# Kernel tuning notes

Hardware: AMD Instinct MI355X
Metric: run time of the kernel (lower is better)

## Reference

```python
import jax, jax.numpy as jnp
import numpy as np
from jax import lax

T, B, D, H = 256, 32, 768, 768


def setup_inputs() -> dict:
    key = jax.random.key(0)
    ks = jax.random.split(key, 8)
    s = 1.0 / np.sqrt(H)
    x = jax.random.normal(ks[0], (T, B, D), dtype=jnp.float32)
    h0 = jax.random.normal(ks[1], (2, B, H), dtype=jnp.float32) * s
    wih_f = jax.random.normal(ks[2], (3 * H, D), dtype=jnp.float32) * s
    whh_f = jax.random.normal(ks[3], (3 * H, H), dtype=jnp.float32) * s
    wih_b = jax.random.normal(ks[4], (3 * H, D), dtype=jnp.float32) * s
    whh_b = jax.random.normal(ks[5], (3 * H, H), dtype=jnp.float32) * s
    bih_f = jnp.zeros((3 * H,), jnp.float32)
    bhh_f = jnp.zeros((3 * H,), jnp.float32)
    bih_b = jnp.zeros((3 * H,), jnp.float32)
    bhh_b = jnp.zeros((3 * H,), jnp.float32)
    # sorted-descending lengths in [T//2, T], as PackedSequence requires
    lengths = jnp.sort(jax.random.randint(ks[6], (B,), T // 2, T + 1))[::-1].astype(jnp.int32)
    return dict(x=x, h0=h0, wih_f=wih_f, whh_f=whh_f, bih_f=bih_f, bhh_f=bhh_f,
                wih_b=wih_b, whh_b=whh_b, bih_b=bih_b, bhh_b=bhh_b, lengths=lengths)


def _gru_scan(x_seq, h0d, Wih, Whh, bih, bhh, mask):
    """Masked GRU scan. x_seq [T,B,D], mask [T,B] bool; hidden frozen where mask is False
    (equivalent to PackedSequence shrinking/growing the active batch)."""
    def step(h, inp):
        x_t, m = inp  # [B,D], [B]
        gx = x_t @ Wih.T + bih          # [B,3H]
        gh = h @ Whh.T + bhh            # [B,3H]
        xr, xz, xn = jnp.split(gx, 3, axis=-1)
        hr, hz, hn = jnp.split(gh, 3, axis=-1)
        r = jax.nn.sigmoid(xr + hr)
        z = jax.nn.sigmoid(xz + hz)
        n = jnp.tanh(xn + r * hn)
        h_new = (1.0 - z) * n + z * h
        h_new = jnp.where(m[:, None], h_new, h)
        return h_new, h_new * m[:, None]  # zero outputs at padded positions
    h_last, outs = lax.scan(step, h0d, (x_seq, mask))
    return outs, h_last


def reference(x, h0, wih_f, whh_f, bih_f, bhh_f, wih_b, whh_b, bih_b, bhh_b, lengths):
    t_idx = jnp.arange(T)[:, None]                 # [T,1]
    mask = t_idx < lengths[None, :]                # [T,B]
    # forward direction
    out_f, h_f = _gru_scan(x, h0[0], wih_f, whh_f, bih_f, bhh_f, mask)
    # reverse direction: flip time, run, flip back
    out_b_rev, h_b = _gru_scan(x[::-1], h0[1], wih_b, whh_b, bih_b, bhh_b, mask[::-1])
    out_b = out_b_rev[::-1]
    outputs = jnp.concatenate([out_f, out_b], axis=-1)  # [T,B,2H], zero beyond length
    h_out = jnp.stack([h_f, h_b], axis=0)                # [2,B,H]
    return outputs, h_out
```

## Files before the change

### kernel.cpp

```cpp
#include <hip/hip_runtime.h>
#include <stdint.h>

typedef unsigned short u16;
typedef _Float16 f16;
typedef __attribute__((ext_vector_type(8))) _Float16 f16x8;
typedef __attribute__((ext_vector_type(4))) float f32x4;
typedef __attribute__((ext_vector_type(4))) unsigned short u16x4;

#define T_SEQ  256
#define BATCH  32
#define DIM    768
#define HID    768
#define G3     2304
#define N_ALL  4608
#define NSLICE 48
#define NBLK   96
#define FLAG_STRIDE 32

__device__ __forceinline__ u16 f2h(float f) {
  return __builtin_bit_cast(u16, (f16)f);
}
__device__ __forceinline__ float h2f(u16 h) {
  return (float)__builtin_bit_cast(f16, h);
}

__device__ __forceinline__ f16x8 load_coh16(const u16* p) {
  f16x8 v;
  asm volatile("global_load_dwordx4 %0, %1, off sc0 sc1" : "=v"(v) : "v"(p));
  return v;
}
__device__ __forceinline__ void store_coh16(u16* p, f16x8 v) {
  asm volatile("global_store_dwordx4 %0, %1, off sc0 sc1" :: "v"(p), "v"(v));
}
__device__ __forceinline__ void wait_vm0() {
  asm volatile("s_waitcnt vmcnt(0)" ::: "memory");
}

__global__ void k_cvt(const float* __restrict__ in, u16* __restrict__ out, int n4) {
  int i = blockIdx.x * blockDim.x + threadIdx.x;
  if (i >= n4) return;
  float4 v = ((const float4*)in)[i];
  u16x4 o;
  o[0] = f2h(v.x); o[1] = f2h(v.y); o[2] = f2h(v.z); o[3] = f2h(v.w);
  ((u16x4*)out)[i] = o;
}

__global__ void k_zero(int* p, int n) {
  int i = blockIdx.x * blockDim.x + threadIdx.x;
  if (i < n) p[i] = 0;
}

__global__ __launch_bounds__(256) void k_gemm(
    const u16* __restrict__ A, const u16* __restrict__ Bw,
    const float* __restrict__ bihf, const float* __restrict__ bihb,
    u16* __restrict__ gx)
{
  __shared__ __align__(16) u16 As[128 * 32];
  __shared__ __align__(16) u16 Bs[128 * 32];
  const int tid  = threadIdx.x;
  const int lane = tid & 63, wave = tid >> 6;
  const int wm = wave >> 1, wn = wave & 1;
  const int m0 = blockIdx.y * 128;
  const int n0 = blockIdx.x * 128;
  const int lr = lane & 15, lk = lane >> 4;
  f32x4 acc[4][4] = {};
  for (int k0 = 0; k0 < DIM; k0 += 32) {
    __syncthreads();
    #pragma unroll
    for (int i = 0; i < 2; ++i) {
      int c = i * 256 + tid;
      int row = c >> 2, kk = (c & 3) * 8;
      *(f16x8*)&As[c * 8] = *(const f16x8*)&A [(size_t)(m0 + row) * DIM + k0 + kk];
      *(f16x8*)&Bs[c * 8] = *(const f16x8*)&Bw[(size_t)(n0 + row) * DIM + k0 + kk];
    }
    __syncthreads();
    f16x8 af[4], bfr[4];
    #pragma unroll
    for (int f = 0; f < 4; ++f) {
      af[f]  = *(const f16x8*)&As[(wm * 64 + f * 16 + lr) * 32 + lk * 8];
      bfr[f] = *(const f16x8*)&Bs[(wn * 64 + f * 16 + lr) * 32 + lk * 8];
    }
    #pragma unroll
    for (int fm = 0; fm < 4; ++fm)
      #pragma unroll
      for (int fn = 0; fn < 4; ++fn)
        acc[fm][fn] = __builtin_amdgcn_mfma_f32_16x16x32_f16(af[fm], bfr[fn], acc[fm][fn], 0, 0, 0);
  }
  #pragma unroll
  for (int fm = 0; fm < 4; ++fm)
    #pragma unroll
    for (int fn = 0; fn < 4; ++fn) {
      int n = n0 + wn * 64 + fn * 16 + lr;
      float bias = (n < G3) ? bihf[n] : bihb[n - G3];
      #pragma unroll
      for (int r = 0; r < 4; ++r) {
        int m = m0 + wm * 64 + fm * 16 + lk * 4 + r;
        gx[(size_t)m * N_ALL + n] = f2h(acc[fm][fn][r] + bias);
      }
    }
}

__global__ __launch_bounds__(256, 1) void k_gru(
    const u16* __restrict__ whh,
    const u16* __restrict__ gx,
    const float* __restrict__ h0,
    const float* __restrict__ bhhf, const float* __restrict__ bhhb,
    const int* __restrict__ lengths,
    u16* __restrict__ hbuf,
    float* __restrict__ out, int* __restrict__ flags)
{
  const int blk   = blockIdx.x;
  const int dir   = blk / NSLICE;
  const int slice = blk % NSLICE;
  const int hbase = slice * 16;
  const int tid = threadIdx.x, lane = tid & 63, wave = tid >> 6;
  const int lr = lane & 15, lk = lane >> 4;
  const int c = hbase + lr;
  const int pollid = tid - 128;
  __shared__ __align__(16) float part[3][2][3][64][4];
  __shared__ __align__(16) u16 hx[32][16];

  f16x8 bw[3][6];
  #pragma unroll
  for (int g = 0; g < 3; ++g)
    #pragma unroll
    for (int ks = 0; ks < 6; ++ks)
      bw[g][ks] = *(const f16x8*)&whh[(size_t)(dir * G3 + g * HID + hbase + lr) * HID
                                      + wave * 192 + ks * 32 + lk * 8];

  float hst[2][4];
  float bh[3] = {0.f, 0.f, 0.f};
  int lenv[2][4];
  u16 g0[2][4], g1[2][4], g2[2][4];
  if (wave == 0) {
    #pragma unroll
    for (int m = 0; m < 2; ++m)
      #pragma unroll
      for (int r = 0; r < 4; ++r) {
        int b = m * 16 + lk * 4 + r;
        float h = h0[(size_t)dir * BATCH * HID + (size_t)b * HID + c];
        hst[m][r] = h;
        lenv[m][r] = lengths[b];
        hx[b][lr] = f2h(h);
      }
    const float* bhp = dir ? bhhb : bhhf;
    #pragma unroll
    for (int g = 0; g < 3; ++g) bh[g] = bhp[g * HID + c];
    asm volatile("s_waitcnt lgkmcnt(0)" ::: "memory");
    {
      f16x8 hv = *(const f16x8*)&hx[lane >> 1][(lane & 1) * 8];
      store_coh16(&hbuf[(size_t)(dir * BATCH + (lane >> 1)) * HID + hbase + (lane & 1) * 8], hv);
    }
    wait_vm0();
    if (lane == 0)
      __hip_atomic_store(&flags[blk * FLAG_STRIDE], 1, __ATOMIC_RELAXED, __HIP_MEMORY_SCOPE_AGENT);
    int t0 = dir ? (T_SEQ - 1) : 0;
    #pragma unroll
    for (int m = 0; m < 2; ++m)
      #pragma unroll
      for (int r = 0; r < 4; ++r) {
        int b = m * 16 + lk * 4 + r;
        size_t off = ((size_t)t0 * BATCH + b) * N_ALL + dir * G3 + c;
        g0[m][r] = gx[off]; g1[m][r] = gx[off + HID]; g2[m][r] = gx[off + 2 * HID];
      }
  }
  if (pollid >= 0 && pollid < NSLICE) {
    const int watch = (dir * NSLICE + pollid) * FLAG_STRIDE;
    while (__hip_atomic_load(&flags[watch], __ATOMIC_RELAXED, __HIP_MEMORY_SCOPE_AGENT) < 1)
      __builtin_amdgcn_s_sleep(1);
  }
  __syncthreads();

  for (int s = 0; s < T_SEQ; ++s) {
    const int par = s & 1;
    const int t = dir ? (T_SEQ - 1 - s) : s;
    const u16* hb = hbuf + (size_t)(par * 2 + dir) * BATCH * HID;
    f16x8 ah[2][6];
    #pragma unroll
    for (int m = 0; m < 2; ++m)
      #pragma unroll
      for (int ks = 0; ks < 6; ++ks)
        ah[m][ks] = load_coh16(&hb[(size_t)(m * 16 + lr) * HID + wave * 192 + ks * 32 + lk * 8]);
    wait_vm0();
    __builtin_amdgcn_sched_barrier(0);
    f32x4 acc[2][3] = {};
    #pragma unroll
    for (int ks = 0; ks < 6; ++ks)
      #pragma unroll
      for (int m = 0; m < 2; ++m)
        #pragma unroll
        for (int g = 0; g < 3; ++g)
          acc[m][g] = __builtin_amdgcn_mfma_f32_16x16x32_f16(ah[m][ks], bw[g][ks], acc[m][g], 0, 0, 0);
    if (wave != 0) {
      #pragma unroll
      for (int m = 0; m < 2; ++m)
        #pragma unroll
        for (int g = 0; g < 3; ++g)
          *(f32x4*)&part[wave - 1][m][g][lane][0] = acc[m][g];
    }
    __syncthreads();
    if (wave == 0) {
      u16* hbn = hbuf + (size_t)((par ^ 1) * 2 + dir) * BATCH * HID;
      float outv[2][4];
      #pragma unroll
      for (int m = 0; m < 2; ++m) {
        f32x4 gh[3];
        #pragma unroll
        for (int g = 0; g < 3; ++g) {
          f32x4 v = acc[m][g];
          #pragma unroll
          for (int w = 0; w < 3; ++w) v += *(const f32x4*)&part[w][m][g][lane][0];
          gh[g] = v;
        }
        #pragma unroll
        for (int r = 0; r < 4; ++r) {
          int b = m * 16 + lk * 4 + r;
          float xr = h2f(g0[m][r]), xz = h2f(g1[m][r]), xn = h2f(g2[m][r]);
          float rg = 1.f / (1.f + __expf(-(xr + gh[0][r] + bh[0])));
          float zg = 1.f / (1.f + __expf(-(xz + gh[1][r] + bh[1])));
          float ng = tanhf(xn + rg * (gh[2][r] + bh[2]));
          float hp = hst[m][r];
          bool msk = t < lenv[m][r];
          float hn2 = msk ? ((1.f - zg) * ng + zg * hp) : hp;
          hst[m][r] = hn2;
          outv[m][r] = msk ? hn2 : 0.f;
          hx[b][lr] = f2h(hn2);
        }
      }
      asm volatile("s_waitcnt lgkmcnt(0)" ::: "memory");
      {
        f16x8 hv = *(const f16x8*)&hx[lane >> 1][(lane & 1) * 8];
        store_coh16(&hbn[(size_t)(lane >> 1) * HID + hbase + (lane & 1) * 8], hv);
      }
      wait_vm0();
      if (lane == 0)
        __hip_atomic_store(&flags[blk * FLAG_STRIDE], s + 2, __ATOMIC_RELAXED, __HIP_MEMORY_SCOPE_AGENT);
      #pragma unroll
      for (int m = 0; m < 2; ++m)
        #pragma unroll
        for (int r = 0; r < 4; ++r) {
          int b = m * 16 + lk * 4 + r;
          __builtin_nontemporal_store(outv[m][r],
              &out[((size_t)t * BATCH + b) * (2 * HID) + (size_t)dir * HID + c]);
        }
      if (s + 1 < T_SEQ) {
        int t2 = dir ? (T_SEQ - 2 - s) : (s + 1);
        #pragma unroll
        for (int m = 0; m < 2; ++m)
          #pragma unroll
          for (int r = 0; r < 4; ++r) {
            int b = m * 16 + lk * 4 + r;
            size_t off = ((size_t)t2 * BATCH + b) * N_ALL + dir * G3 + c;
            g0[m][r] = gx[off]; g1[m][r] = gx[off + HID]; g2[m][r] = gx[off + 2 * HID];
          }
      }
    }
    if (pollid >= 0 && pollid < NSLICE) {
      const int watch = (dir * NSLICE + pollid) * FLAG_STRIDE;
      while (__hip_atomic_load(&flags[watch], __ATOMIC_RELAXED, __HIP_MEMORY_SCOPE_AGENT) < s + 2)
        __builtin_amdgcn_s_sleep(1);
    }
    __syncthreads();
  }
  if (wave == 0) {
    #pragma unroll
    for (int m = 0; m < 2; ++m)
      #pragma unroll
      for (int r = 0; r < 4; ++r) {
        int b = m * 16 + lk * 4 + r;
        out[(size_t)T_SEQ * BATCH * 2 * HID + (size_t)dir * BATCH * HID + (size_t)b * HID + c] = hst[m][r];
      }
  }
}

extern "C" void kernel_launch(void* const* d_in, const int* in_sizes, int n_in,
                              void* d_out, int out_size, void* d_ws, size_t ws_size,
                              hipStream_t stream) {
  const float* x     = (const float*)d_in[0];
  const float* h0    = (const float*)d_in[1];
  const float* wihf  = (const float*)d_in[2];
  const float* whhf  = (const float*)d_in[3];
  const float* bihf  = (const float*)d_in[4];
  const float* bhhf  = (const float*)d_in[5];
  const float* wihb  = (const float*)d_in[6];
  const float* whhb  = (const float*)d_in[7];
  const float* bihb  = (const float*)d_in[8];
  const float* bhhb  = (const float*)d_in[9];
  const int* lengths = (const int*)d_in[10];
  float* out = (float*)d_out;
  char* ws = (char*)d_ws;

  u16* xh    = (u16*)(ws + 0);
  u16* wih_h = (u16*)(ws + 12582912);
  u16* whh_h = (u16*)(ws + 19660800);
  u16* gx    = (u16*)(ws + 26738688);
  u16* hbuf  = (u16*)(ws + 102236160);
  int* flags = (int*)(ws + 102432768);

  k_cvt<<<6144, 256, 0, stream>>>(x, xh, 1572864);
  k_cvt<<<1728, 256, 0, stream>>>(wihf, wih_h,            442368);
  k_cvt<<<1728, 256, 0, stream>>>(wihb, wih_h + 1769472,  442368);
  k_cvt<<<1728, 256, 0, stream>>>(whhf, whh_h,            442368);
  k_cvt<<<1728, 256, 0, stream>>>(whhb, whh_h + 1769472,  442368);
  k_zero<<<12, 256, 0, stream>>>(flags, NBLK * FLAG_STRIDE);
  k_gemm<<<dim3(36, 64), 256, 0, stream>>>(xh, wih_h, bihf, bihb, gx);
  k_gru<<<NBLK, 256, 0, stream>>>(whh_h, gx, h0, bhhf, bhhb, lengths, hbuf, out, flags);
}
```

Baseline: 1.421 ms.

## Fuse fp32-to-fp16 conversion into input GEMM and trim GRU step overheads

The input projection GEMM now reads fp32 x and both W_ih matrices directly and packs them to fp16 while filling shared memory. This removes three conversion kernels and the round trip of the fp16 copies through global memory. Alongside that, the flag-zeroing kernel becomes a hipMemsetAsync, and tanhf is replaced by an exp-based formula. Explicit vmcnt waits are added after the gx prefetch loads in the recurrent kernel. The GEMM re-converts each tile on every load, which adds ALU work and doubles the bytes read per tile, and the exp-based tanh can lose accuracy.

Result: faster. 1.301 ms (-8.5%).

```diff
diff --git a/kernel.cpp b/kernel.cpp
--- a/kernel.cpp
+++ b/kernel.cpp
@@ -2,10 +2,13 @@
 #include <stdint.h>
 
 typedef unsigned short u16;
+typedef unsigned int u32;
 typedef _Float16 f16;
+typedef __attribute__((ext_vector_type(2))) __fp16 h16x2;
 typedef __attribute__((ext_vector_type(8))) _Float16 f16x8;
 typedef __attribute__((ext_vector_type(4))) float f32x4;
 typedef __attribute__((ext_vector_type(4))) unsigned short u16x4;
+typedef __attribute__((ext_vector_type(4))) unsigned int u32x4;
 
 #define T_SEQ  256
 #define BATCH  32
@@ -35,6 +38,18 @@
 __device__ __forceinline__ void wait_vm0() {
   asm volatile("s_waitcnt vmcnt(0)" ::: "memory");
 }
+__device__ __forceinline__ u32 pkrtz(float a, float b) {
+  h16x2 p = __builtin_amdgcn_cvt_pkrtz(a, b);
+  return __builtin_bit_cast(u32, p);
+}
+__device__ __forceinline__ f16x8 cvt8(float4 a, float4 b) {
+  u32x4 r;
+  r.x = pkrtz(a.x, a.y);
+  r.y = pkrtz(a.z, a.w);
+  r.z = pkrtz(b.x, b.y);
+  r.w = pkrtz(b.z, b.w);
+  return __builtin_bit_cast(f16x8, r);
+}
 
 __global__ void k_cvt(const float* __restrict__ in, u16* __restrict__ out, int n4) {
   int i = blockIdx.x * blockDim.x + threadIdx.x;
@@ -45,13 +60,9 @@
   ((u16x4*)out)[i] = o;
 }
 
-__global__ void k_zero(int* p, int n) {
-  int i = blockIdx.x * blockDim.x + threadIdx.x;
-  if (i < n) p[i] = 0;
-}
-
 __global__ __launch_bounds__(256) void k_gemm(
-    const u16* __restrict__ A, const u16* __restrict__ Bw,
+    const float* __restrict__ X, const float* __restrict__ Wf,
+    const float* __restrict__ Wb,
     const float* __restrict__ bihf, const float* __restrict__ bihb,
     u16* __restrict__ gx)
 {
@@ -68,10 +79,13 @@
     __syncthreads();
     #pragma unroll
     for (int i = 0; i < 2; ++i) {
-      int c = i * 256 + tid;
-      int row = c >> 2, kk = (c & 3) * 8;
-      *(f16x8*)&As[c * 8] = *(const f16x8*)&A [(size_t)(m0 + row) * DIM + k0 + kk];
-      *(f16x8*)&Bs[c * 8] = *(const f16x8*)&Bw[(size_t)(n0 + row) * DIM + k0 + kk];
+      int cidx = i * 256 + tid;
+      int row = cidx >> 2, kk = (cidx & 3) * 8;
+      const float* ap = &X[(size_t)(m0 + row) * DIM + k0 + kk];
+      *(f16x8*)&As[cidx * 8] = cvt8(*(const float4*)ap, *(const float4*)(ap + 4));
+      int n = n0 + row;
+      const float* bp = (n < G3 ? &Wf[(size_t)n * DIM] : &Wb[(size_t)(n - G3) * DIM]) + k0 + kk;
+      *(f16x8*)&Bs[cidx * 8] = cvt8(*(const float4*)bp, *(const float4*)(bp + 4));
     }
     __syncthreads();
     f16x8 af[4], bfr[4];
@@ -163,6 +177,7 @@
         size_t off = ((size_t)t0 * BATCH + b) * N_ALL + dir * G3 + c;
         g0[m][r] = gx[off]; g1[m][r] = gx[off + HID]; g2[m][r] = gx[off + 2 * HID];
       }
+    wait_vm0();
   }
   if (pollid >= 0 && pollid < NSLICE) {
     const int watch = (dir * NSLICE + pollid) * FLAG_STRIDE;
@@ -218,13 +233,14 @@
           float xr = h2f(g0[m][r]), xz = h2f(g1[m][r]), xn = h2f(g2[m][r]);
           float rg = 1.f / (1.f + __expf(-(xr + gh[0][r] + bh[0])));
           float zg = 1.f / (1.f + __expf(-(xz + gh[1][r] + bh[1])));
-          float ng = tanhf(xn + rg * (gh[2][r] + bh[2]));
+          float e2 = __expf(2.f * (xn + rg * (gh[2][r] + bh[2])));
+          float ng = 1.f - 2.f / (e2 + 1.f);
           float hp = hst[m][r];
           bool msk = t < lenv[m][r];
-          float hn2 = msk ? ((1.f - zg) * ng + zg * hp) : hp;
-          hst[m][r] = hn2;
-          outv[m][r] = msk ? hn2 : 0.f;
-          hx[b][lr] = f2h(hn2);
+          float hn = msk ? ((1.f - zg) * ng + zg * hp) : hp;
+          hst[m][r] = hn;
+          outv[m][r] = msk ? hn : 0.f;
+          hx[b][lr] = f2h(hn);
         }
       }
       asm volatile("s_waitcnt lgkmcnt(0)" ::: "memory");
@@ -254,6 +270,7 @@
             g0[m][r] = gx[off]; g1[m][r] = gx[off + HID]; g2[m][r] = gx[off + 2 * HID];
           }
       }
+      wait_vm0();
     }
     if (pollid >= 0 && pollid < NSLICE) {
       const int watch = (dir * NSLICE + pollid) * FLAG_STRIDE;
@@ -290,19 +307,14 @@
   float* out = (float*)d_out;
   char* ws = (char*)d_ws;
 
-  u16* xh    = (u16*)(ws + 0);
-  u16* wih_h = (u16*)(ws + 12582912);
-  u16* whh_h = (u16*)(ws + 19660800);
-  u16* gx    = (u16*)(ws + 26738688);
-  u16* hbuf  = (u16*)(ws + 102236160);
-  int* flags = (int*)(ws + 102432768);
-
-  k_cvt<<<6144, 256, 0, stream>>>(x, xh, 1572864);
-  k_cvt<<<1728, 256, 0, stream>>>(wihf, wih_h,            442368);
-  k_cvt<<<1728, 256, 0, stream>>>(wihb, wih_h + 1769472,  442368);
+  int* flags = (int*)(ws + 0);
+  u16* whh_h = (u16*)(ws + 24576);
+  u16* hbuf  = (u16*)(ws + 7102464);
+  u16* gx    = (u16*)(ws + 7299072);
+
   k_cvt<<<1728, 256, 0, stream>>>(whhf, whh_h,            442368);
   k_cvt<<<1728, 256, 0, stream>>>(whhb, whh_h + 1769472,  442368);
-  k_zero<<<12, 256, 0, stream>>>(flags, NBLK * FLAG_STRIDE);
-  k_gemm<<<dim3(36, 64), 256, 0, stream>>>(xh, wih_h, bihf, bihb, gx);
+  (void)hipMemsetAsync(flags, 0, NBLK * FLAG_STRIDE * sizeof(int), stream);
+  k_gemm<<<dim3(36, 64), 256, 0, stream>>>(x, wihf, wihb, bihf, bihb, gx);
   k_gru<<<NBLK, 256, 0, stream>>>(whh_h, gx, h0, bhhf, bhhb, lengths, hbuf, out, flags);
 }
```
